# Performance work log

Measured on AMD Instinct MI355X. Metric: run time of the kernel, lower is better.

## Reference

```python
import jax, jax.numpy as jnp
import numpy as np

# Static block sizes (2-layer neighbor-sampled blocks, fanout=10, 10k seed genes)
N_SRC1, N_DST1 = 1_210_000, 110_000
N_SRC2, N_DST2 = 110_000, 10_000
E1, E2 = 1_100_000, 100_000
IN_DIM, HID_DIM, OUT_DIM = 128, 256, 128


def setup_inputs() -> dict:
    key = jax.random.key(0)
    ks = jax.random.split(key, 12)
    feat = jax.random.normal(ks[0], (N_SRC1, IN_DIM), dtype=jnp.float32)
    src_idx1 = jax.random.randint(ks[1], (E1,), 0, N_SRC1)
    dst_idx1 = jax.random.randint(ks[2], (E1,), 0, N_DST1)
    src_idx2 = jax.random.randint(ks[3], (E2,), 0, N_SRC2)
    dst_idx2 = jax.random.randint(ks[4], (E2,), 0, N_DST2)
    s1 = 1.0 / np.sqrt(IN_DIM)
    s2 = 1.0 / np.sqrt(HID_DIM)
    W1 = jax.random.uniform(ks[5], (IN_DIM, HID_DIM), jnp.float32, -s1, s1)
    b1 = jnp.zeros((HID_DIM,), jnp.float32)
    attn1 = jax.random.uniform(ks[6], (HID_DIM, 1), jnp.float32, -s2, s2)
    W2 = jax.random.uniform(ks[7], (HID_DIM, OUT_DIM), jnp.float32, -s2, s2)
    b2 = jnp.zeros((OUT_DIM,), jnp.float32)
    s3 = 1.0 / np.sqrt(OUT_DIM)
    attn2 = jax.random.uniform(ks[8], (OUT_DIM, 1), jnp.float32, -s3, s3)
    return {"feat": feat, "W1": W1, "b1": b1, "attn1": attn1,
            "W2": W2, "b2": b2, "attn2": attn2,
            "src_idx1": src_idx1, "dst_idx1": dst_idx1,
            "src_idx2": src_idx2, "dst_idx2": dst_idx2}


def _gcn_gated_layer(h, src_idx, dst_idx, n_src, n_dst, W, b, attn_w):
    """DGL GraphConv(norm='both') on a block + sigmoid gene-attention gate."""
    ones = jnp.ones(src_idx.shape, jnp.float32)
    out_deg = jnp.clip(jax.ops.segment_sum(ones, src_idx, num_segments=n_src), 1.0)
    in_deg = jnp.clip(jax.ops.segment_sum(ones, dst_idx, num_segments=n_dst), 1.0)
    hs = h * jax.lax.rsqrt(out_deg)[:, None]            # src-side norm
    agg = jax.ops.segment_sum(hs[src_idx], dst_idx, num_segments=n_dst)
    hd = agg * jax.lax.rsqrt(in_deg)[:, None]           # dst-side norm
    hd = hd @ W + b                                     # GraphConv linear
    alpha = jax.nn.sigmoid(hd @ attn_w)                 # (n_dst, 1) gate
    return hd * alpha, alpha


def reference(feat, W1, b1, attn1, W2, b2, attn2,
              src_idx1, dst_idx1, src_idx2, dst_idx2):
    h, _ = _gcn_gated_layer(feat, src_idx1, dst_idx1, N_SRC1, N_DST1, W1, b1, attn1)
    h, alpha = _gcn_gated_layer(h, src_idx2, dst_idx2, N_SRC2, N_DST2, W2, b2, attn2)
    return h, alpha
```

## Files before the change

kernel.cpp:

```cpp
#include <hip/hip_runtime.h>
#include <cstddef>
#include <cstdint>

#define N_SRC1 1210000
#define N_DST1 110000
#define N_SRC2 110000
#define N_DST2 10000
#define E1 1100000
#define E2 100000
#define IN_DIM 128
#define HID_DIM 256
#define OUT_DIM 128

__global__ __launch_bounds__(256) void count_kernel(const int* __restrict__ src,
                                                    const int* __restrict__ dst,
                                                    float* __restrict__ outdeg,
                                                    int* __restrict__ cnt, int E) {
    int i = blockIdx.x * 256 + threadIdx.x;
    if (i < E) {
        unsafeAtomicAdd(&outdeg[src[i]], 1.0f);
        atomicAdd(&cnt[dst[i]], 1);
    }
}

__global__ __launch_bounds__(256) void rsqrt_kernel(float* __restrict__ p, int n) {
    int i = blockIdx.x * 256 + threadIdx.x;
    if (i < n) p[i] = rsqrtf(fmaxf(p[i], 1.0f));
}

__global__ __launch_bounds__(1024) void scan_part(const int* __restrict__ cnt,
                                                  int* __restrict__ offs,
                                                  int* __restrict__ bsum, int n) {
    __shared__ int smem[1024];
    int i = blockIdx.x * 1024 + threadIdx.x;
    int v = (i < n) ? cnt[i] : 0;
    smem[threadIdx.x] = v;
    __syncthreads();
    #pragma unroll
    for (int off = 1; off < 1024; off <<= 1) {
        int t = (threadIdx.x >= off) ? smem[threadIdx.x - off] : 0;
        __syncthreads();
        smem[threadIdx.x] += t;
        __syncthreads();
    }
    if (i < n) offs[i] = smem[threadIdx.x] - v;
    if (threadIdx.x == 1023) bsum[blockIdx.x] = smem[1023];
}

__global__ __launch_bounds__(1024) void scan_bsum(int* __restrict__ bsum,
                                                  int* __restrict__ offs_end, int nb) {
    __shared__ int smem[1024];
    int v = (threadIdx.x < nb) ? bsum[threadIdx.x] : 0;
    smem[threadIdx.x] = v;
    __syncthreads();
    #pragma unroll
    for (int off = 1; off < 1024; off <<= 1) {
        int t = (threadIdx.x >= off) ? smem[threadIdx.x - off] : 0;
        __syncthreads();
        smem[threadIdx.x] += t;
        __syncthreads();
    }
    if (threadIdx.x < nb) bsum[threadIdx.x] = smem[threadIdx.x] - v;
    if (threadIdx.x == nb - 1) *offs_end = smem[threadIdx.x];
}

__global__ __launch_bounds__(1024) void scan_add(int* __restrict__ offs,
                                                 int* __restrict__ cursor,
                                                 const int* __restrict__ bsum, int n) {
    int i = blockIdx.x * 1024 + threadIdx.x;
    if (i < n) {
        int o = offs[i] + bsum[blockIdx.x];
        offs[i] = o;
        cursor[i] = o;
    }
}

__global__ __launch_bounds__(256) void fill_kernel(const int* __restrict__ src,
                                                   const int* __restrict__ dst,
                                                   int* __restrict__ cursor,
                                                   int* __restrict__ elist, int E) {
    int i = blockIdx.x * 256 + threadIdx.x;
    if (i < E) {
        int pos = atomicAdd(&cursor[dst[i]], 1);
        elist[pos] = src[i];
    }
}

__global__ __launch_bounds__(256) void gather1_kernel(const float* __restrict__ feat,
                                                      const int* __restrict__ elist,
                                                      const int* __restrict__ offs,
                                                      const float* __restrict__ rs_out,
                                                      float* __restrict__ agg, int n_dst) {
    int d = blockIdx.x * 4 + (threadIdx.x >> 6);
    if (d >= n_dst) return;
    int lane = threadIdx.x & 63;
    int beg = offs[d], end = offs[d + 1];
    float2 acc = make_float2(0.f, 0.f);
    int j = beg;
    for (; j + 4 <= end; j += 4) {
        int s0 = elist[j + 0];
        int s1 = elist[j + 1];
        int s2 = elist[j + 2];
        int s3 = elist[j + 3];
        float c0 = rs_out[s0], c1 = rs_out[s1], c2 = rs_out[s2], c3 = rs_out[s3];
        float2 v0 = ((const float2*)(feat + (size_t)s0 * IN_DIM))[lane];
        float2 v1 = ((const float2*)(feat + (size_t)s1 * IN_DIM))[lane];
        float2 v2 = ((const float2*)(feat + (size_t)s2 * IN_DIM))[lane];
        float2 v3 = ((const float2*)(feat + (size_t)s3 * IN_DIM))[lane];
        acc.x += v0.x * c0 + v1.x * c1 + v2.x * c2 + v3.x * c3;
        acc.y += v0.y * c0 + v1.y * c1 + v2.y * c2 + v3.y * c3;
    }
    for (; j < end; ++j) {
        int s = elist[j];
        float sc = rs_out[s];
        float2 v = ((const float2*)(feat + (size_t)s * IN_DIM))[lane];
        acc.x += v.x * sc;
        acc.y += v.y * sc;
    }
    float rin = rsqrtf(fmaxf((float)(end - beg), 1.f));
    acc.x *= rin; acc.y *= rin;
    ((float2*)(agg + (size_t)d * IN_DIM))[lane] = acc;
}

__global__ __launch_bounds__(256) void gather2_kernel(const float* __restrict__ h1,
                                                      const int* __restrict__ elist,
                                                      const int* __restrict__ offs,
                                                      const float* __restrict__ rs_out,
                                                      float* __restrict__ agg, int n_dst) {
    int d = blockIdx.x * 4 + (threadIdx.x >> 6);
    if (d >= n_dst) return;
    int lane = threadIdx.x & 63;
    int beg = offs[d], end = offs[d + 1];
    float4 acc = make_float4(0.f, 0.f, 0.f, 0.f);
    int j = beg;
    for (; j + 4 <= end; j += 4) {
        int s0 = elist[j + 0];
        int s1 = elist[j + 1];
        int s2 = elist[j + 2];
        int s3 = elist[j + 3];
        float c0 = rs_out[s0], c1 = rs_out[s1], c2 = rs_out[s2], c3 = rs_out[s3];
        float4 v0 = ((const float4*)(h1 + (size_t)s0 * HID_DIM))[lane];
        float4 v1 = ((const float4*)(h1 + (size_t)s1 * HID_DIM))[lane];
        float4 v2 = ((const float4*)(h1 + (size_t)s2 * HID_DIM))[lane];
        float4 v3 = ((const float4*)(h1 + (size_t)s3 * HID_DIM))[lane];
        acc.x += v0.x * c0 + v1.x * c1 + v2.x * c2 + v3.x * c3;
        acc.y += v0.y * c0 + v1.y * c1 + v2.y * c2 + v3.y * c3;
        acc.z += v0.z * c0 + v1.z * c1 + v2.z * c2 + v3.z * c3;
        acc.w += v0.w * c0 + v1.w * c1 + v2.w * c2 + v3.w * c3;
    }
    for (; j < end; ++j) {
        int s = elist[j];
        float sc = rs_out[s];
        float4 v = ((const float4*)(h1 + (size_t)s * HID_DIM))[lane];
        acc.x += v.x * sc;
        acc.y += v.y * sc;
        acc.z += v.z * sc;
        acc.w += v.w * sc;
    }
    float rin = rsqrtf(fmaxf((float)(end - beg), 1.f));
    acc.x *= rin; acc.y *= rin; acc.z *= rin; acc.w *= rin;
    ((float4*)(agg + (size_t)d * HID_DIM))[lane] = acc;
}

__global__ __launch_bounds__(512) void gemm1_gate(const float* __restrict__ agg,
                                                  const float* __restrict__ W,
                                                  const float* __restrict__ bias,
                                                  const float* __restrict__ attn,
                                                  float* __restrict__ h1, int M) {
    __shared__ float As[64][IN_DIM + 4];
    __shared__ float Bs[32][HID_DIM];
    const int t = threadIdx.x;
    const int row0 = blockIdx.x * 64;
    const int col = t & 63;
    const int rbase = (t >> 6) * 8;

    #pragma unroll
    for (int i = 0; i < 4; ++i) {
        int idx = t + i * 512;
        int r = idx >> 5, c4 = idx & 31;
        int row = row0 + r;
        float4 v = make_float4(0.f, 0.f, 0.f, 0.f);
        if (row < M) v = ((const float4*)(agg + (size_t)row * IN_DIM))[c4];
        *(float4*)&As[r][c4 * 4] = v;
    }

    float4 acc[8];
    #pragma unroll
    for (int rr = 0; rr < 8; ++rr) acc[rr] = make_float4(0.f, 0.f, 0.f, 0.f);

    for (int kc = 0; kc < 4; ++kc) {
        __syncthreads();
        #pragma unroll
        for (int i = 0; i < 4; ++i) {
            int idx = t + i * 512;
            int kk = idx >> 6, c4 = idx & 63;
            *(float4*)&Bs[kk][c4 * 4] = ((const float4*)(W + (size_t)(kc * 32 + kk) * HID_DIM))[c4];
        }
        __syncthreads();
        #pragma unroll 2
        for (int k4 = 0; k4 < 8; ++k4) {
            int kk = k4 * 4;
            float4 b0 = *(float4*)&Bs[kk + 0][col * 4];
            float4 b1v = *(float4*)&Bs[kk + 1][col * 4];
            float4 b2v = *(float4*)&Bs[kk + 2][col * 4];
            float4 b3v = *(float4*)&Bs[kk + 3][col * 4];
            int ka = kc * 32 + kk;
            #pragma unroll
            for (int rr = 0; rr < 8; ++rr) {
                float4 a = *(const float4*)&As[rbase + rr][ka];
                acc[rr].x += a.x * b0.x + a.y * b1v.x + a.z * b2v.x + a.w * b3v.x;
                acc[rr].y += a.x * b0.y + a.y * b1v.y + a.z * b2v.y + a.w * b3v.y;
                acc[rr].z += a.x * b0.z + a.y * b1v.z + a.z * b2v.z + a.w * b3v.z;
                acc[rr].w += a.x * b0.w + a.y * b1v.w + a.z * b2v.w + a.w * b3v.w;
            }
        }
    }

    float4 bb = *(const float4*)&bias[col * 4];
    float4 at = *(const float4*)&attn[col * 4];
    #pragma unroll
    for (int rr = 0; rr < 8; ++rr) {
        int row = row0 + rbase + rr;
        float4 v = acc[rr];
        v.x += bb.x; v.y += bb.y; v.z += bb.z; v.w += bb.w;
        float p = v.x * at.x + v.y * at.y + v.z * at.z + v.w * at.w;
        p += __shfl_down(p, 32);
        p += __shfl_down(p, 16);
        p += __shfl_down(p, 8);
        p += __shfl_down(p, 4);
        p += __shfl_down(p, 2);
        p += __shfl_down(p, 1);
        p = __shfl(p, 0);
        float alpha = 1.f / (1.f + expf(-p));
        v.x *= alpha; v.y *= alpha; v.z *= alpha; v.w *= alpha;
        if (row < M) *(float4*)&h1[(size_t)row * HID_DIM + col * 4] = v;
    }
}

__global__ __launch_bounds__(256) void gemm2_gate(const float* __restrict__ agg,
                                                  const float* __restrict__ W,
                                                  const float* __restrict__ bias,
                                                  const float* __restrict__ attn,
                                                  float* __restrict__ out_h,
                                                  float* __restrict__ out_alpha, int M) {
    __shared__ float As[32][HID_DIM + 4];
    __shared__ float Bs[32][OUT_DIM];
    const int t = threadIdx.x;
    const int row0 = blockIdx.x * 32;
    const int col = t & 63;
    const int rbase = (t >> 6) * 8;

    #pragma unroll
    for (int i = 0; i < 8; ++i) {
        int idx = t + i * 256;
        int r = idx >> 6, c4 = idx & 63;
        int row = row0 + r;
        float4 v = make_float4(0.f, 0.f, 0.f, 0.f);
        if (row < M) v = ((const float4*)(agg + (size_t)row * HID_DIM))[c4];
        *(float4*)&As[r][c4 * 4] = v;
    }

    float2 acc[8];
    #pragma unroll
    for (int rr = 0; rr < 8; ++rr) acc[rr] = make_float2(0.f, 0.f);

    for (int kc = 0; kc < 8; ++kc) {
        __syncthreads();
        #pragma unroll
        for (int i = 0; i < 4; ++i) {
            int idx = t + i * 256;
            int kk = idx >> 5, c4 = idx & 31;
            *(float4*)&Bs[kk][c4 * 4] = ((const float4*)(W + (size_t)(kc * 32 + kk) * OUT_DIM))[c4];
        }
        __syncthreads();
        #pragma unroll
        for (int k4 = 0; k4 < 8; ++k4) {
            int kk = k4 * 4;
            float2 b0 = *(float2*)&Bs[kk + 0][col * 2];
            float2 b1v = *(float2*)&Bs[kk + 1][col * 2];
            float2 b2v = *(float2*)&Bs[kk + 2][col * 2];
            float2 b3v = *(float2*)&Bs[kk + 3][col * 2];
            int ka = kc * 32 + kk;
            #pragma unroll
            for (int rr = 0; rr < 8; ++rr) {
                float4 a = *(const float4*)&As[rbase + rr][ka];
                acc[rr].x += a.x * b0.x + a.y * b1v.x + a.z * b2v.x + a.w * b3v.x;
                acc[rr].y += a.x * b0.y + a.y * b1v.y + a.z * b2v.y + a.w * b3v.y;
            }
        }
    }

    float2 bb = *(const float2*)&bias[col * 2];
    float2 at = *(const float2*)&attn[col * 2];
    #pragma unroll
    for (int rr = 0; rr < 8; ++rr) {
        int row = row0 + rbase + rr;
        float2 v = acc[rr];
        v.x += bb.x; v.y += bb.y;
        float p = v.x * at.x + v.y * at.y;
        p += __shfl_down(p, 32);
        p += __shfl_down(p, 16);
        p += __shfl_down(p, 8);
        p += __shfl_down(p, 4);
        p += __shfl_down(p, 2);
        p += __shfl_down(p, 1);
        p = __shfl(p, 0);
        float alpha = 1.f / (1.f + expf(-p));
        v.x *= alpha; v.y *= alpha;
        if (row < M) {
            *(float2*)&out_h[(size_t)row * OUT_DIM + col * 2] = v;
            if (col == 0) out_alpha[row] = alpha;
        }
    }
}

extern "C" void kernel_launch(void* const* d_in, const int* in_sizes, int n_in,
                              void* d_out, int out_size, void* d_ws, size_t ws_size,
                              hipStream_t stream) {
    const float* feat  = (const float*)d_in[0];
    const float* W1    = (const float*)d_in[1];
    const float* b1    = (const float*)d_in[2];
    const float* attn1 = (const float*)d_in[3];
    const float* W2    = (const float*)d_in[4];
    const float* b2    = (const float*)d_in[5];
    const float* attn2 = (const float*)d_in[6];
    const int* src1 = (const int*)d_in[7];
    const int* dst1 = (const int*)d_in[8];
    const int* src2 = (const int*)d_in[9];
    const int* dst2 = (const int*)d_in[10];
    float* out = (float*)d_out;

    float* ws = (float*)d_ws;
    float* outdeg1 = ws;
    float* outdeg2 = outdeg1 + N_SRC1;
    int*   cnt1    = (int*)(outdeg2 + N_SRC2);
    int*   cnt2    = cnt1 + N_DST1;
    int*   offs1   = cnt2 + N_DST2;
    int*   cursor1 = offs1 + N_DST1 + 1;
    int*   offs2   = cursor1 + N_DST1;
    int*   cursor2 = offs2 + N_DST2 + 1;
    int*   elist1  = cursor2 + N_DST2;
    int*   elist2  = elist1 + E1;
    float* agg1    = (float*)(elist2 + E2);
    float* agg2    = agg1 + (size_t)N_DST1 * IN_DIM;
    float* h1      = agg2 + (size_t)N_DST2 * HID_DIM;
    int*   bsum1   = (int*)(h1 + (size_t)N_DST1 * HID_DIM);
    int*   bsum2   = bsum1 + 128;

    const size_t zero_bytes = ((size_t)N_SRC1 + N_SRC2 + N_DST1 + N_DST2) * 4;
    hipMemsetAsync(d_ws, 0, zero_bytes, stream);

    count_kernel<<<(E1 + 255) / 256, 256, 0, stream>>>(src1, dst1, outdeg1, cnt1, E1);
    count_kernel<<<(E2 + 255) / 256, 256, 0, stream>>>(src2, dst2, outdeg2, cnt2, E2);
    rsqrt_kernel<<<(N_SRC1 + N_SRC2 + 255) / 256, 256, 0, stream>>>(outdeg1, N_SRC1 + N_SRC2);

    const int nb1 = (N_DST1 + 1023) / 1024;
    const int nb2 = (N_DST2 + 1023) / 1024;
    scan_part<<<nb1, 1024, 0, stream>>>(cnt1, offs1, bsum1, N_DST1);
    scan_bsum<<<1, 1024, 0, stream>>>(bsum1, offs1 + N_DST1, nb1);
    scan_add<<<nb1, 1024, 0, stream>>>(offs1, cursor1, bsum1, N_DST1);
    scan_part<<<nb2, 1024, 0, stream>>>(cnt2, offs2, bsum2, N_DST2);
    scan_bsum<<<1, 1024, 0, stream>>>(bsum2, offs2 + N_DST2, nb2);
    scan_add<<<nb2, 1024, 0, stream>>>(offs2, cursor2, bsum2, N_DST2);

    fill_kernel<<<(E1 + 255) / 256, 256, 0, stream>>>(src1, dst1, cursor1, elist1, E1);
    fill_kernel<<<(E2 + 255) / 256, 256, 0, stream>>>(src2, dst2, cursor2, elist2, E2);

    gather1_kernel<<<(N_DST1 + 3) / 4, 256, 0, stream>>>(feat, elist1, offs1, outdeg1, agg1, N_DST1);
    gemm1_gate<<<(N_DST1 + 63) / 64, 512, 0, stream>>>(agg1, W1, b1, attn1, h1, N_DST1);
    gather2_kernel<<<(N_DST2 + 3) / 4, 256, 0, stream>>>(h1, elist2, offs2, outdeg2, agg2, N_DST2);
    gemm2_gate<<<(N_DST2 + 31) / 32, 256, 0, stream>>>(agg2, W2, b2, attn2,
                                                       out, out + (size_t)N_DST2 * OUT_DIM, N_DST2);
}
```

Baseline: 1.171 ms.

## Fuse layer-1 gather into GEMM, merge per-layer setup kernels, inline rsqrt

```diff
diff --git a/kernel.cpp b/kernel.cpp
--- a/kernel.cpp
+++ b/kernel.cpp
@@ -12,27 +12,36 @@
 #define HID_DIM 256
 #define OUT_DIM 128
 
-__global__ __launch_bounds__(256) void count_kernel(const int* __restrict__ src,
-                                                    const int* __restrict__ dst,
-                                                    float* __restrict__ outdeg,
-                                                    int* __restrict__ cnt, int E) {
+__global__ __launch_bounds__(256) void count_both(const int* __restrict__ src1,
+                                                  const int* __restrict__ dst1,
+                                                  const int* __restrict__ src2,
+                                                  const int* __restrict__ dst2,
+                                                  float* __restrict__ outdeg1,
+                                                  int* __restrict__ cnt1,
+                                                  float* __restrict__ outdeg2,
+                                                  int* __restrict__ cnt2) {
     int i = blockIdx.x * 256 + threadIdx.x;
-    if (i < E) {
-        unsafeAtomicAdd(&outdeg[src[i]], 1.0f);
-        atomicAdd(&cnt[dst[i]], 1);
-    }
-}
-
-__global__ __launch_bounds__(256) void rsqrt_kernel(float* __restrict__ p, int n) {
-    int i = blockIdx.x * 256 + threadIdx.x;
-    if (i < n) p[i] = rsqrtf(fmaxf(p[i], 1.0f));
-}
-
-__global__ __launch_bounds__(1024) void scan_part(const int* __restrict__ cnt,
-                                                  int* __restrict__ offs,
-                                                  int* __restrict__ bsum, int n) {
+    if (i < E1) {
+        unsafeAtomicAdd(&outdeg1[src1[i]], 1.0f);
+        atomicAdd(&cnt1[dst1[i]], 1);
+    } else if (i < E1 + E2) {
+        int k = i - E1;
+        unsafeAtomicAdd(&outdeg2[src2[k]], 1.0f);
+        atomicAdd(&cnt2[dst2[k]], 1);
+    }
+}
+
+__global__ __launch_bounds__(1024) void scan_part_both(const int* __restrict__ cnt1,
+                                                       int* __restrict__ offs1,
+                                                       int* __restrict__ bsum1,
+                                                       const int* __restrict__ cnt2,
+                                                       int* __restrict__ offs2,
+                                                       int* __restrict__ bsum2, int nb1) {
+    const int* cnt; int* offs; int* bsum; int n; int lb;
+    if ((int)blockIdx.x < nb1) { cnt = cnt1; offs = offs1; bsum = bsum1; n = N_DST1; lb = blockIdx.x; }
+    else                       { cnt = cnt2; offs = offs2; bsum = bsum2; n = N_DST2; lb = blockIdx.x - nb1; }
     __shared__ int smem[1024];
-    int i = blockIdx.x * 1024 + threadIdx.x;
+    int i = lb * 1024 + threadIdx.x;
     int v = (i < n) ? cnt[i] : 0;
     smem[threadIdx.x] = v;
     __syncthreads();
@@ -44,13 +53,18 @@
         __syncthreads();
     }
     if (i < n) offs[i] = smem[threadIdx.x] - v;
-    if (threadIdx.x == 1023) bsum[blockIdx.x] = smem[1023];
-}
-
-__global__ __launch_bounds__(1024) void scan_bsum(int* __restrict__ bsum,
-                                                  int* __restrict__ offs_end, int nb) {
+    if (threadIdx.x == 1023) bsum[lb] = smem[1023];
+}
+
+__global__ __launch_bounds__(1024) void scan_bsum_both(int* __restrict__ bsum1,
+                                                       int* __restrict__ end1, int nb1,
+                                                       int* __restrict__ bsum2,
+                                                       int* __restrict__ end2, int nb2) {
+    int* bsum; int* oend; int nb;
+    if (blockIdx.x == 0) { bsum = bsum1; oend = end1; nb = nb1; }
+    else                 { bsum = bsum2; oend = end2; nb = nb2; }
     __shared__ int smem[1024];
-    int v = (threadIdx.x < nb) ? bsum[threadIdx.x] : 0;
+    int v = ((int)threadIdx.x < nb) ? bsum[threadIdx.x] : 0;
     smem[threadIdx.x] = v;
     __syncthreads();
     #pragma unroll
@@ -60,128 +74,97 @@
         smem[threadIdx.x] += t;
         __syncthreads();
     }
-    if (threadIdx.x < nb) bsum[threadIdx.x] = smem[threadIdx.x] - v;
-    if (threadIdx.x == nb - 1) *offs_end = smem[threadIdx.x];
-}
-
-__global__ __launch_bounds__(1024) void scan_add(int* __restrict__ offs,
-                                                 int* __restrict__ cursor,
-                                                 const int* __restrict__ bsum, int n) {
-    int i = blockIdx.x * 1024 + threadIdx.x;
+    if ((int)threadIdx.x < nb) bsum[threadIdx.x] = smem[threadIdx.x] - v;
+    if ((int)threadIdx.x == nb - 1) *oend = smem[threadIdx.x];
+}
+
+__global__ __launch_bounds__(1024) void scan_add_both(int* __restrict__ offs1,
+                                                      int* __restrict__ cursor1,
+                                                      const int* __restrict__ bsum1,
+                                                      int* __restrict__ offs2,
+                                                      int* __restrict__ cursor2,
+                                                      const int* __restrict__ bsum2, int nb1) {
+    int* offs; int* cursor; const int* bsum; int n; int lb;
+    if ((int)blockIdx.x < nb1) { offs = offs1; cursor = cursor1; bsum = bsum1; n = N_DST1; lb = blockIdx.x; }
+    else                       { offs = offs2; cursor = cursor2; bsum = bsum2; n = N_DST2; lb = blockIdx.x - nb1; }
+    int i = lb * 1024 + threadIdx.x;
     if (i < n) {
-        int o = offs[i] + bsum[blockIdx.x];
+        int o = offs[i] + bsum[lb];
         offs[i] = o;
         cursor[i] = o;
     }
 }
 
-__global__ __launch_bounds__(256) void fill_kernel(const int* __restrict__ src,
-                                                   const int* __restrict__ dst,
-                                                   int* __restrict__ cursor,
-                                                   int* __restrict__ elist, int E) {
+__global__ __launch_bounds__(256) void fill_both(const int* __restrict__ src1,
+                                                 const int* __restrict__ dst1,
+                                                 int* __restrict__ cursor1,
+                                                 int* __restrict__ elist1,
+                                                 const int* __restrict__ src2,
+                                                 const int* __restrict__ dst2,
+                                                 int* __restrict__ cursor2,
+                                                 int* __restrict__ elist2) {
     int i = blockIdx.x * 256 + threadIdx.x;
-    if (i < E) {
-        int pos = atomicAdd(&cursor[dst[i]], 1);
-        elist[pos] = src[i];
-    }
-}
-
-__global__ __launch_bounds__(256) void gather1_kernel(const float* __restrict__ feat,
-                                                      const int* __restrict__ elist,
-                                                      const int* __restrict__ offs,
-                                                      const float* __restrict__ rs_out,
-                                                      float* __restrict__ agg, int n_dst) {
-    int d = blockIdx.x * 4 + (threadIdx.x >> 6);
-    if (d >= n_dst) return;
-    int lane = threadIdx.x & 63;
-    int beg = offs[d], end = offs[d + 1];
-    float2 acc = make_float2(0.f, 0.f);
-    int j = beg;
-    for (; j + 4 <= end; j += 4) {
-        int s0 = elist[j + 0];
-        int s1 = elist[j + 1];
-        int s2 = elist[j + 2];
-        int s3 = elist[j + 3];
-        float c0 = rs_out[s0], c1 = rs_out[s1], c2 = rs_out[s2], c3 = rs_out[s3];
-        float2 v0 = ((const float2*)(feat + (size_t)s0 * IN_DIM))[lane];
-        float2 v1 = ((const float2*)(feat + (size_t)s1 * IN_DIM))[lane];
-        float2 v2 = ((const float2*)(feat + (size_t)s2 * IN_DIM))[lane];
-        float2 v3 = ((const float2*)(feat + (size_t)s3 * IN_DIM))[lane];
-        acc.x += v0.x * c0 + v1.x * c1 + v2.x * c2 + v3.x * c3;
-        acc.y += v0.y * c0 + v1.y * c1 + v2.y * c2 + v3.y * c3;
-    }
-    for (; j < end; ++j) {
-        int s = elist[j];
-        float sc = rs_out[s];
-        float2 v = ((const float2*)(feat + (size_t)s * IN_DIM))[lane];
-        acc.x += v.x * sc;
-        acc.y += v.y * sc;
-    }
-    float rin = rsqrtf(fmaxf((float)(end - beg), 1.f));
-    acc.x *= rin; acc.y *= rin;
-    ((float2*)(agg + (size_t)d * IN_DIM))[lane] = acc;
-}
-
-__global__ __launch_bounds__(256) void gather2_kernel(const float* __restrict__ h1,
-                                                      const int* __restrict__ elist,
-                                                      const int* __restrict__ offs,
-                                                      const float* __restrict__ rs_out,
-                                                      float* __restrict__ agg, int n_dst) {
-    int d = blockIdx.x * 4 + (threadIdx.x >> 6);
-    if (d >= n_dst) return;
-    int lane = threadIdx.x & 63;
-    int beg = offs[d], end = offs[d + 1];
-    float4 acc = make_float4(0.f, 0.f, 0.f, 0.f);
-    int j = beg;
-    for (; j + 4 <= end; j += 4) {
-        int s0 = elist[j + 0];
-        int s1 = elist[j + 1];
-        int s2 = elist[j + 2];
-        int s3 = elist[j + 3];
-        float c0 = rs_out[s0], c1 = rs_out[s1], c2 = rs_out[s2], c3 = rs_out[s3];
-        float4 v0 = ((const float4*)(h1 + (size_t)s0 * HID_DIM))[lane];
-        float4 v1 = ((const float4*)(h1 + (size_t)s1 * HID_DIM))[lane];
-        float4 v2 = ((const float4*)(h1 + (size_t)s2 * HID_DIM))[lane];
-        float4 v3 = ((const float4*)(h1 + (size_t)s3 * HID_DIM))[lane];
-        acc.x += v0.x * c0 + v1.x * c1 + v2.x * c2 + v3.x * c3;
-        acc.y += v0.y * c0 + v1.y * c1 + v2.y * c2 + v3.y * c3;
-        acc.z += v0.z * c0 + v1.z * c1 + v2.z * c2 + v3.z * c3;
-        acc.w += v0.w * c0 + v1.w * c1 + v2.w * c2 + v3.w * c3;
-    }
-    for (; j < end; ++j) {
-        int s = elist[j];
-        float sc = rs_out[s];
-        float4 v = ((const float4*)(h1 + (size_t)s * HID_DIM))[lane];
-        acc.x += v.x * sc;
-        acc.y += v.y * sc;
-        acc.z += v.z * sc;
-        acc.w += v.w * sc;
-    }
-    float rin = rsqrtf(fmaxf((float)(end - beg), 1.f));
-    acc.x *= rin; acc.y *= rin; acc.z *= rin; acc.w *= rin;
-    ((float4*)(agg + (size_t)d * HID_DIM))[lane] = acc;
-}
-
-__global__ __launch_bounds__(512) void gemm1_gate(const float* __restrict__ agg,
-                                                  const float* __restrict__ W,
-                                                  const float* __restrict__ bias,
-                                                  const float* __restrict__ attn,
-                                                  float* __restrict__ h1, int M) {
+    if (i < E1) {
+        int pos = atomicAdd(&cursor1[dst1[i]], 1);
+        elist1[pos] = src1[i];
+    } else if (i < E1 + E2) {
+        int k = i - E1;
+        int pos = atomicAdd(&cursor2[dst2[k]], 1);
+        elist2[pos] = src2[k];
+    }
+}
+
+__global__ __launch_bounds__(512) void gather_gemm1_gate(const float* __restrict__ feat,
+                                                         const int* __restrict__ elist,
+                                                         const int* __restrict__ offs,
+                                                         const float* __restrict__ outdeg,
+                                                         const float* __restrict__ W,
+                                                         const float* __restrict__ bias,
+                                                         const float* __restrict__ attn,
+                                                         float* __restrict__ h1, int M) {
     __shared__ float As[64][IN_DIM + 4];
     __shared__ float Bs[32][HID_DIM];
     const int t = threadIdx.x;
     const int row0 = blockIdx.x * 64;
-    const int col = t & 63;
-    const int rbase = (t >> 6) * 8;
-
-    #pragma unroll
-    for (int i = 0; i < 4; ++i) {
-        int idx = t + i * 512;
-        int r = idx >> 5, c4 = idx & 31;
-        int row = row0 + r;
-        float4 v = make_float4(0.f, 0.f, 0.f, 0.f);
-        if (row < M) v = ((const float4*)(agg + (size_t)row * IN_DIM))[c4];
-        *(float4*)&As[r][c4 * 4] = v;
+    const int lane = t & 63;
+    const int wid = t >> 6;
+    const int col = lane;
+    const int rbase = wid * 8;
+
+    for (int rr = 0; rr < 8; ++rr) {
+        int r = rbase + rr;
+        int d = row0 + r;
+        float2 acc = make_float2(0.f, 0.f);
+        if (d < M) {
+            int beg = offs[d], end = offs[d + 1];
+            int j = beg;
+            for (; j + 4 <= end; j += 4) {
+                int s0 = elist[j + 0];
+                int s1 = elist[j + 1];
+                int s2 = elist[j + 2];
+                int s3 = elist[j + 3];
+                float c0 = rsqrtf(fmaxf(outdeg[s0], 1.f));
+                float c1 = rsqrtf(fmaxf(outdeg[s1], 1.f));
+                float c2 = rsqrtf(fmaxf(outdeg[s2], 1.f));
+                float c3 = rsqrtf(fmaxf(outdeg[s3], 1.f));
+                float2 v0 = ((const float2*)(feat + (size_t)s0 * IN_DIM))[lane];
+                float2 v1 = ((const float2*)(feat + (size_t)s1 * IN_DIM))[lane];
+                float2 v2 = ((const float2*)(feat + (size_t)s2 * IN_DIM))[lane];
+                float2 v3 = ((const float2*)(feat + (size_t)s3 * IN_DIM))[lane];
+                acc.x += v0.x * c0 + v1.x * c1 + v2.x * c2 + v3.x * c3;
+                acc.y += v0.y * c0 + v1.y * c1 + v2.y * c2 + v3.y * c3;
+            }
+            for (; j < end; ++j) {
+                int s = elist[j];
+                float sc = rsqrtf(fmaxf(outdeg[s], 1.f));
+                float2 v = ((const float2*)(feat + (size_t)s * IN_DIM))[lane];
+                acc.x += v.x * sc;
+                acc.y += v.y * sc;
+            }
+            float rin = rsqrtf(fmaxf((float)(end - beg), 1.f));
+            acc.x *= rin; acc.y *= rin;
+        }
+        *(float2*)&As[r][lane * 2] = acc;
     }
 
     float4 acc[8];
@@ -235,6 +218,49 @@
         v.x *= alpha; v.y *= alpha; v.z *= alpha; v.w *= alpha;
         if (row < M) *(float4*)&h1[(size_t)row * HID_DIM + col * 4] = v;
     }
+}
+
+__global__ __launch_bounds__(256) void gather2_kernel(const float* __restrict__ h1,
+                                                      const int* __restrict__ elist,
+                                                      const int* __restrict__ offs,
+                                                      const float* __restrict__ outdeg,
+                                                      float* __restrict__ agg, int n_dst) {
+    int d = blockIdx.x * 4 + (threadIdx.x >> 6);
+    if (d >= n_dst) return;
+    int lane = threadIdx.x & 63;
+    int beg = offs[d], end = offs[d + 1];
+    float4 acc = make_float4(0.f, 0.f, 0.f, 0.f);
+    int j = beg;
+    for (; j + 4 <= end; j += 4) {
+        int s0 = elist[j + 0];
+        int s1 = elist[j + 1];
+        int s2 = elist[j + 2];
+        int s3 = elist[j + 3];
+        float c0 = rsqrtf(fmaxf(outdeg[s0], 1.f));
+        float c1 = rsqrtf(fmaxf(outdeg[s1], 1.f));
+        float c2 = rsqrtf(fmaxf(outdeg[s2], 1.f));
+        float c3 = rsqrtf(fmaxf(outdeg[s3], 1.f));
+        float4 v0 = ((const float4*)(h1 + (size_t)s0 * HID_DIM))[lane];
+        float4 v1 = ((const float4*)(h1 + (size_t)s1 * HID_DIM))[lane];
+        float4 v2 = ((const float4*)(h1 + (size_t)s2 * HID_DIM))[lane];
+        float4 v3 = ((const float4*)(h1 + (size_t)s3 * HID_DIM))[lane];
+        acc.x += v0.x * c0 + v1.x * c1 + v2.x * c2 + v3.x * c3;
+        acc.y += v0.y * c0 + v1.y * c1 + v2.y * c2 + v3.y * c3;
+        acc.z += v0.z * c0 + v1.z * c1 + v2.z * c2 + v3.z * c3;
+        acc.w += v0.w * c0 + v1.w * c1 + v2.w * c2 + v3.w * c3;
+    }
+    for (; j < end; ++j) {
+        int s = elist[j];
+        float sc = rsqrtf(fmaxf(outdeg[s], 1.f));
+        float4 v = ((const float4*)(h1 + (size_t)s * HID_DIM))[lane];
+        acc.x += v.x * sc;
+        acc.y += v.y * sc;
+        acc.z += v.z * sc;
+        acc.w += v.w * sc;
+    }
+    float rin = rsqrtf(fmaxf((float)(end - beg), 1.f));
+    acc.x *= rin; acc.y *= rin; acc.z *= rin; acc.w *= rin;
+    ((float4*)(agg + (size_t)d * HID_DIM))[lane] = acc;
 }
 
 __global__ __launch_bounds__(256) void gemm2_gate(const float* __restrict__ agg,
@@ -341,8 +367,7 @@
     int*   cursor2 = offs2 + N_DST2 + 1;
     int*   elist1  = cursor2 + N_DST2;
     int*   elist2  = elist1 + E1;
-    float* agg1    = (float*)(elist2 + E2);
-    float* agg2    = agg1 + (size_t)N_DST1 * IN_DIM;
+    float* agg2    = (float*)(elist2 + E2);
     float* h1      = agg2 + (size_t)N_DST2 * HID_DIM;
     int*   bsum1   = (int*)(h1 + (size_t)N_DST1 * HID_DIM);
     int*   bsum2   = bsum1 + 128;
@@ -350,24 +375,20 @@
     const size_t zero_bytes = ((size_t)N_SRC1 + N_SRC2 + N_DST1 + N_DST2) * 4;
     hipMemsetAsync(d_ws, 0, zero_bytes, stream);
 
-    count_kernel<<<(E1 + 255) / 256, 256, 0, stream>>>(src1, dst1, outdeg1, cnt1, E1);
-    count_kernel<<<(E2 + 255) / 256, 256, 0, stream>>>(src2, dst2, outdeg2, cnt2, E2);
-    rsqrt_kernel<<<(N_SRC1 + N_SRC2 + 255) / 256, 256, 0, stream>>>(outdeg1, N_SRC1 + N_SRC2);
+    count_both<<<(E1 + E2 + 255) / 256, 256, 0, stream>>>(src1, dst1, src2, dst2,
+                                                          outdeg1, cnt1, outdeg2, cnt2);
 
     const int nb1 = (N_DST1 + 1023) / 1024;
     const int nb2 = (N_DST2 + 1023) / 1024;
-    scan_part<<<nb1, 1024, 0, stream>>>(cnt1, offs1, bsum1, N_DST1);
-    scan_bsum<<<1, 1024, 0, stream>>>(bsum1, offs1 + N_DST1, nb1);
-    scan_add<<<nb1, 1024, 0, stream>>>(offs1, cursor1, bsum1, N_DST1);
-    scan_part<<<nb2, 1024, 0, stream>>>(cnt2, offs2, bsum2, N_DST2);
-    scan_bsum<<<1, 1024, 0, stream>>>(bsum2, offs2 + N_DST2, nb2);
-    scan_add<<<nb2, 1024, 0, stream>>>(offs2, cursor2, bsum2, N_DST2);
-
-    fill_kernel<<<(E1 + 255) / 256, 256, 0, stream>>>(src1, dst1, cursor1, elist1, E1);
-    fill_kernel<<<(E2 + 255) / 256, 256, 0, stream>>>(src2, dst2, cursor2, elist2, E2);
-
-    gather1_kernel<<<(N_DST1 + 3) / 4, 256, 0, stream>>>(feat, elist1, offs1, outdeg1, agg1, N_DST1);
-    gemm1_gate<<<(N_DST1 + 63) / 64, 512, 0, stream>>>(agg1, W1, b1, attn1, h1, N_DST1);
+    scan_part_both<<<nb1 + nb2, 1024, 0, stream>>>(cnt1, offs1, bsum1, cnt2, offs2, bsum2, nb1);
+    scan_bsum_both<<<2, 1024, 0, stream>>>(bsum1, offs1 + N_DST1, nb1, bsum2, offs2 + N_DST2, nb2);
+    scan_add_both<<<nb1 + nb2, 1024, 0, stream>>>(offs1, cursor1, bsum1, offs2, cursor2, bsum2, nb1);
+
+    fill_both<<<(E1 + E2 + 255) / 256, 256, 0, stream>>>(src1, dst1, cursor1, elist1,
+                                                         src2, dst2, cursor2, elist2);
+
+    gather_gemm1_gate<<<(N_DST1 + 63) / 64, 512, 0, stream>>>(feat, elist1, offs1, outdeg1,
+                                                              W1, b1, attn1, h1, N_DST1);
     gather2_kernel<<<(N_DST2 + 3) / 4, 256, 0, stream>>>(h1, elist2, offs2, outdeg2, agg2, N_DST2);
     gemm2_gate<<<(N_DST2 + 31) / 32, 256, 0, stream>>>(agg2, W2, b2, attn2,
                                                        out, out + (size_t)N_DST2 * OUT_DIM, N_DST2);
```

After: 1.184 ms. No clear change (+1.1%).
